# Kernel optimization log

Hardware: AMD Instinct MI355X
Metric: run time of the kernel (lower is better)

The kernel has to match this reference:

```python
import jax, jax.numpy as jnp
import numpy as np

B, T, C = 4, 2048, 1024
QH = 4            # n_q_heads
D = C // QH       # per-head dim = 256
EPS = 1e-5


def setup_inputs() -> dict:
    key = jax.random.key(0)
    k1, k2, k3 = jax.random.split(key, 3)
    residual = jax.random.normal(k1, (B, T, C), dtype=jnp.float32)
    # scale weights ~ Xavier-ish so relu(score)^2 stays numerically sane
    w_fc = jax.random.normal(k2, (C, C), dtype=jnp.float32) * (1.0 / np.sqrt(C))
    w_proj = jax.random.normal(k3, (C, C), dtype=jnp.float32) * (1.0 / np.sqrt(C))
    ln_g = jnp.ones((C,), dtype=jnp.float32)
    ln_b = jnp.zeros((C,), dtype=jnp.float32)
    return {"residual": residual, "w_fc": w_fc, "w_proj": w_proj,
            "ln_g": ln_g, "ln_b": ln_b}


def _layernorm(x, g, b):
    mu = jnp.mean(x, axis=-1, keepdims=True)
    var = jnp.mean(jnp.square(x - mu), axis=-1, keepdims=True)
    return (x - mu) * jax.lax.rsqrt(var + EPS) * g + b


def reference(residual, w_fc, w_proj, ln_g, ln_b):
    Bx, Tx, Cx = residual.shape
    x = _layernorm(residual, ln_g, ln_b)
    # q: (B, QH, T, D)
    q = x.reshape(Bx, Tx, QH, D).transpose(0, 2, 1, 3)
    # keys: rows of w_fc chopped into 4C kv entries of dim D, shared across heads
    k = w_fc.reshape(-1, D)          # (S, D), S = 4C
    # values: columns of w_proj (i.e. w_proj^T rows) chopped the same way
    v = w_proj.T.reshape(-1, D)      # (S, D)
    scores = jnp.einsum('bhtd,sd->bhts', q, k)
    # softmax(log(relusq(score))) then *exp(lse) == plain relu(score)^2 weights
    p = jnp.square(jax.nn.relu(scores))
    out = jnp.einsum('bhts,sd->bhtd', p, v)
    out = out.transpose(0, 2, 1, 3).reshape(Bx, Tx, Cx)
    return residual + out
```

## Files before the change

### kernel.cpp

```cpp
#include <hip/hip_runtime.h>
#include <hip/hip_bf16.h>

typedef __attribute__((ext_vector_type(8))) short bf16x8;
typedef __attribute__((ext_vector_type(4))) float f32x4;

#define C_    1024
#define MROWS 32768
#define D_    256
#define S_TOT 4096
#define SCH   32
#define NCH   (S_TOT / SCH)

__device__ __forceinline__ unsigned short f2bf(float f) {
  union { float f; unsigned int u; } v; v.f = f;
  unsigned int u = v.u;
  u += 0x7fffu + ((u >> 16) & 1u);
  return (unsigned short)(u >> 16);
}

__device__ __forceinline__ void async16(const void* g, void* l) {
  __builtin_amdgcn_global_load_lds(
      (const __attribute__((address_space(1))) unsigned int*)g,
      (__attribute__((address_space(3))) unsigned int*)l, 16, 0, 0);
}

__global__ __launch_bounds__(256) void ln_kernel(const float* __restrict__ res,
                                                 const float* __restrict__ g,
                                                 const float* __restrict__ b,
                                                 unsigned short* __restrict__ xq) {
  int wave = threadIdx.x >> 6, lane = threadIdx.x & 63;
  int row = blockIdx.x * 4 + wave;
  const float* r = res + (size_t)row * C_;
  float4 x[4];
  float s = 0.f, s2 = 0.f;
  #pragma unroll
  for (int i = 0; i < 4; ++i) {
    x[i] = *(const float4*)(r + i * 256 + lane * 4);
    s  += x[i].x + x[i].y + x[i].z + x[i].w;
    s2 += x[i].x * x[i].x + x[i].y * x[i].y + x[i].z * x[i].z + x[i].w * x[i].w;
  }
  #pragma unroll
  for (int off = 32; off > 0; off >>= 1) {
    s  += __shfl_xor(s, off, 64);
    s2 += __shfl_xor(s2, off, 64);
  }
  float mu  = s * (1.0f / C_);
  float var = s2 * (1.0f / C_) - mu * mu;
  float rs  = rsqrtf(var + 1e-5f);
  #pragma unroll
  for (int i = 0; i < 4; ++i) {
    int c = i * 256 + lane * 4;
    float4 gg = *(const float4*)(g + c);
    float4 bb = *(const float4*)(b + c);
    unsigned short o[4];
    o[0] = f2bf((x[i].x - mu) * rs * gg.x + bb.x);
    o[1] = f2bf((x[i].y - mu) * rs * gg.y + bb.y);
    o[2] = f2bf((x[i].z - mu) * rs * gg.z + bb.z);
    o[3] = f2bf((x[i].w - mu) * rs * gg.w + bb.w);
    *(ushort4*)(xq + (size_t)row * C_ + c) = *(ushort4*)o;
  }
}

__global__ __launch_bounds__(256) void prep_k(const float* __restrict__ wfc,
                                              unsigned short* __restrict__ kq) {
  int t = blockIdx.x * 256 + threadIdx.x;
  int lane = t & 63;
  int sn  = (t >> 6) & 1;
  int kc  = (t >> 7) & 7;
  int sc2 = t >> 10;
  int s = sc2 * 32 + sn * 16 + (lane & 15);
  int d = kc * 32 + (lane >> 4) * 8;
  const float* src = wfc + (size_t)s * D_ + d;
  float4 a = *(const float4*)src;
  float4 b = *(const float4*)(src + 4);
  unsigned short o[8] = { f2bf(a.x), f2bf(a.y), f2bf(a.z), f2bf(a.w),
                          f2bf(b.x), f2bf(b.y), f2bf(b.z), f2bf(b.w) };
  *(uint4*)(kq + (size_t)t * 8) = *(uint4*)o;
}

__global__ __launch_bounds__(256) void prep_v(const float* __restrict__ wproj,
                                              unsigned short* __restrict__ vq) {
  __shared__ unsigned short tile[8192];
  int b = blockIdx.x;
  int tid = threadIdx.x;
  int c0 = b * 8;
  #pragma unroll
  for (int it = 0; it < 4; ++it) {
    int row = it * 256 + tid;
    const float* src = wproj + (size_t)row * C_ + c0;
    float4 a = *(const float4*)src;
    float4 bb = *(const float4*)(src + 4);
    unsigned short* dst = &tile[row * 8];
    dst[0] = f2bf(a.x);  dst[1] = f2bf(a.y);  dst[2] = f2bf(a.z);  dst[3] = f2bf(a.w);
    dst[4] = f2bf(bb.x); dst[5] = f2bf(bb.y); dst[6] = f2bf(bb.z); dst[7] = f2bf(bb.w);
  }
  __syncthreads();
  #pragma unroll
  for (int it = 0; it < 4; ++it) {
    int slot = it * 256 + tid;
    int lane = slot & 63;
    int dn   = slot >> 6;
    int d = dn * 16 + (lane & 15);
    int sl0 = (lane >> 4) * 8;
    unsigned short o[8];
    #pragma unroll
    for (int j = 0; j < 8; ++j) {
      int sl = sl0 + j;
      o[j] = tile[((sl & 3) * 256 + d) * 8 + (sl >> 2)];
    }
    *(uint4*)(vq + (size_t)b * 8192 + (size_t)slot * 8) = *(uint4*)o;
  }
}

__global__ __launch_bounds__(512, 2) void mlpmha_main(
    const unsigned short* __restrict__ xq,
    const unsigned short* __restrict__ kq,
    const unsigned short* __restrict__ vq,
    const float* __restrict__ res,
    float* __restrict__ out) {
  __shared__ unsigned short ldsK[2][8192];
  __shared__ unsigned short ldsV[8192];
  __shared__ unsigned short ldsP[128][36];

  int tid  = threadIdx.x;
  int wave = tid >> 6;
  int lane = tid & 63;
  int l16  = lane & 15;
  int quad = lane >> 4;
  int wgM  = blockIdx.x * 128;

  int mi = wave & 3, si = wave >> 2;
  int ni = wave & 3, mi2 = wave >> 2;

  bf16x8 qf[2][8];
  #pragma unroll
  for (int mt = 0; mt < 2; ++mt) {
    const unsigned short* qr =
        xq + (size_t)(wgM + mi * 32 + mt * 16 + l16) * D_ + quad * 8;
    #pragma unroll
    for (int kc = 0; kc < 8; ++kc) qf[mt][kc] = *(const bf16x8*)(qr + kc * 32);
  }

  f32x4 acc[4][4];
  #pragma unroll
  for (int i = 0; i < 4; ++i)
    #pragma unroll
    for (int j = 0; j < 4; ++j) acc[i][j] = (f32x4){0.f, 0.f, 0.f, 0.f};

  int soff = tid * 8;

  {
    const unsigned short* kg = kq + soff;
    async16(kg, &ldsK[0][soff]);
    async16(kg + 4096, &ldsK[0][soff + 4096]);
  }
  __syncthreads();

  for (int sc = 0; sc < NCH; ++sc) {
    int cur = sc & 1;

    {
      const unsigned short* vg = vq + (size_t)sc * 8192 + soff;
      async16(vg, &ldsV[soff]);
      async16(vg + 4096, &ldsV[soff + 4096]);
    }

    f32x4 sacc[2];
    sacc[0] = (f32x4){0.f, 0.f, 0.f, 0.f};
    sacc[1] = (f32x4){0.f, 0.f, 0.f, 0.f};
    #pragma unroll
    for (int kc = 0; kc < 8; ++kc) {
      bf16x8 kb = *(const bf16x8*)&ldsK[cur][(kc * 2 + si) * 512 + lane * 8];
      #pragma unroll
      for (int mt = 0; mt < 2; ++mt)
        sacc[mt] = __builtin_amdgcn_mfma_f32_16x16x32_bf16(qf[mt][kc], kb, sacc[mt], 0, 0, 0);
    }

    #pragma unroll
    for (int mt = 0; mt < 2; ++mt)
      #pragma unroll
      for (int r = 0; r < 4; ++r) {
        float v = sacc[mt][r];
        v = v > 0.f ? v * v : 0.f;
        ldsP[mi * 32 + mt * 16 + quad * 4 + r][si * 16 + l16] = f2bf(v);
      }

    __syncthreads();

    if (sc + 1 < NCH) {
      const unsigned short* kg = kq + (size_t)(sc + 1) * 8192 + soff;
      async16(kg, &ldsK[1 - cur][soff]);
      async16(kg + 4096, &ldsK[1 - cur][soff + 4096]);
    }

    {
      bf16x8 vb[4];
      #pragma unroll
      for (int dnl = 0; dnl < 4; ++dnl)
        vb[dnl] = *(const bf16x8*)&ldsV[((ni * 4 + dnl) * 64 + lane) * 8];
      #pragma unroll
      for (int mt2 = 0; mt2 < 4; ++mt2) {
        const unsigned short* pp = &ldsP[mi2 * 64 + mt2 * 16 + l16][quad * 8];
        union { ushort4 h[2]; bf16x8 v; } pu;
        pu.h[0] = *(const ushort4*)pp;
        pu.h[1] = *(const ushort4*)(pp + 4);
        bf16x8 pa = pu.v;
        #pragma unroll
        for (int dnl = 0; dnl < 4; ++dnl)
          acc[mt2][dnl] = __builtin_amdgcn_mfma_f32_16x16x32_bf16(pa, vb[dnl], acc[mt2][dnl], 0, 0, 0);
      }
    }

    __syncthreads();
  }

  #pragma unroll
  for (int mt2 = 0; mt2 < 4; ++mt2)
    #pragma unroll
    for (int r = 0; r < 4; ++r) {
      size_t row = (size_t)(wgM + mi2 * 64 + mt2 * 16 + quad * 4 + r) * D_;
      #pragma unroll
      for (int dnl = 0; dnl < 4; ++dnl) {
        size_t idx = row + ni * 64 + dnl * 16 + l16;
        out[idx] = res[idx] + acc[mt2][dnl][r];
      }
    }
}

extern "C" void kernel_launch(void* const* d_in, const int* in_sizes, int n_in,
                              void* d_out, int out_size, void* d_ws, size_t ws_size,
                              hipStream_t stream) {
  const float* res   = (const float*)d_in[0];
  const float* wfc   = (const float*)d_in[1];
  const float* wproj = (const float*)d_in[2];
  const float* g     = (const float*)d_in[3];
  const float* b     = (const float*)d_in[4];
  float* out = (float*)d_out;

  unsigned short* xq = (unsigned short*)d_ws;
  unsigned short* kq = xq + (size_t)MROWS * D_;
  unsigned short* vq = kq + (size_t)S_TOT * D_;

  ln_kernel<<<2048, 256, 0, stream>>>(res, g, b, xq);
  prep_k<<<512, 256, 0, stream>>>(wfc, kq);
  prep_v<<<128, 256, 0, stream>>>(wproj, vq);
  mlpmha_main<<<256, 512, 0, stream>>>(xq, kq, vq, res, out);
}
```

Before: 243.0 us.

## Software-pipeline scores and PV phases with triple-buffered P and register V

Restructures the main loop so the score MFMA for chunk s+1 overlaps the P·V MFMA for chunk s. P gets three LDS buffers, which cuts the loop to one barrier per chunk instead of two. V fragments are loaded straight from global memory into registers, double-buffered, instead of being staged through LDS. This is meant to remove barrier stalls and LDS traffic, at the cost of more registers and V reads from global/L2 that are exposed to latency.

```diff
diff --git a/kernel.cpp b/kernel.cpp
--- a/kernel.cpp
+++ b/kernel.cpp
@@ -119,8 +119,7 @@
     const float* __restrict__ res,
     float* __restrict__ out) {
   __shared__ unsigned short ldsK[2][8192];
-  __shared__ unsigned short ldsV[8192];
-  __shared__ unsigned short ldsP[128][36];
+  __shared__ unsigned short ldsP[3][128][36];
 
   int tid  = threadIdx.x;
   int wave = tid >> 6;
@@ -149,22 +148,23 @@
 
   int soff = tid * 8;
 
-  {
-    const unsigned short* kg = kq + soff;
-    async16(kg, &ldsK[0][soff]);
-    async16(kg + 4096, &ldsK[0][soff + 4096]);
-  }
-  __syncthreads();
-
-  for (int sc = 0; sc < NCH; ++sc) {
+  bf16x8 vbA[4], vbB[4];
+
+  auto load_v = [&](int sc, bf16x8 (&vb)[4]) {
+    const unsigned short* vg = vq + (size_t)sc * 8192;
+    #pragma unroll
+    for (int dnl = 0; dnl < 4; ++dnl)
+      vb[dnl] = *(const bf16x8*)(vg + ((ni * 4 + dnl) * 64 + lane) * 8);
+  };
+
+  auto issueK = [&](int sc, int buf) {
+    const unsigned short* kg = kq + (size_t)sc * 8192 + soff;
+    async16(kg, &ldsK[buf][soff]);
+    async16(kg + 4096, &ldsK[buf][soff + 4096]);
+  };
+
+  auto scores_phase = [&](int sc, int pw) {
     int cur = sc & 1;
-
-    {
-      const unsigned short* vg = vq + (size_t)sc * 8192 + soff;
-      async16(vg, &ldsV[soff]);
-      async16(vg + 4096, &ldsV[soff + 4096]);
-    }
-
     f32x4 sacc[2];
     sacc[0] = (f32x4){0.f, 0.f, 0.f, 0.f};
     sacc[1] = (f32x4){0.f, 0.f, 0.f, 0.f};
@@ -175,44 +175,63 @@
       for (int mt = 0; mt < 2; ++mt)
         sacc[mt] = __builtin_amdgcn_mfma_f32_16x16x32_bf16(qf[mt][kc], kb, sacc[mt], 0, 0, 0);
     }
-
     #pragma unroll
     for (int mt = 0; mt < 2; ++mt)
       #pragma unroll
       for (int r = 0; r < 4; ++r) {
         float v = sacc[mt][r];
         v = v > 0.f ? v * v : 0.f;
-        ldsP[mi * 32 + mt * 16 + quad * 4 + r][si * 16 + l16] = f2bf(v);
+        ldsP[pw][mi * 32 + mt * 16 + quad * 4 + r][si * 16 + l16] = f2bf(v);
       }
-
+  };
+
+  auto pv_phase = [&](int pr, bf16x8 (&vb)[4]) {
+    #pragma unroll
+    for (int mt2 = 0; mt2 < 4; ++mt2) {
+      const unsigned short* pp = &ldsP[pr][mi2 * 64 + mt2 * 16 + l16][quad * 8];
+      union { ushort4 h[2]; bf16x8 v; } pu;
+      pu.h[0] = *(const ushort4*)pp;
+      pu.h[1] = *(const ushort4*)(pp + 4);
+      bf16x8 pa = pu.v;
+      #pragma unroll
+      for (int dnl = 0; dnl < 4; ++dnl)
+        acc[mt2][dnl] = __builtin_amdgcn_mfma_f32_16x16x32_bf16(pa, vb[dnl], acc[mt2][dnl], 0, 0, 0);
+    }
+  };
+
+  issueK(0, 0);
+  issueK(1, 1);
+  load_v(0, vbA);
+  __syncthreads();
+
+  scores_phase(0, 0);
+  __syncthreads();
+  issueK(2, 0);
+
+  int prev = 0;
+  int nxt  = 1;
+
+  for (int sc = 1; sc < NCH - 1; sc += 2) {
+    load_v(sc, vbB);
+    scores_phase(sc, nxt);
     __syncthreads();
-
-    if (sc + 1 < NCH) {
-      const unsigned short* kg = kq + (size_t)(sc + 1) * 8192 + soff;
-      async16(kg, &ldsK[1 - cur][soff]);
-      async16(kg + 4096, &ldsK[1 - cur][soff + 4096]);
-    }
-
-    {
-      bf16x8 vb[4];
-      #pragma unroll
-      for (int dnl = 0; dnl < 4; ++dnl)
-        vb[dnl] = *(const bf16x8*)&ldsV[((ni * 4 + dnl) * 64 + lane) * 8];
-      #pragma unroll
-      for (int mt2 = 0; mt2 < 4; ++mt2) {
-        const unsigned short* pp = &ldsP[mi2 * 64 + mt2 * 16 + l16][quad * 8];
-        union { ushort4 h[2]; bf16x8 v; } pu;
-        pu.h[0] = *(const ushort4*)pp;
-        pu.h[1] = *(const ushort4*)(pp + 4);
-        bf16x8 pa = pu.v;
-        #pragma unroll
-        for (int dnl = 0; dnl < 4; ++dnl)
-          acc[mt2][dnl] = __builtin_amdgcn_mfma_f32_16x16x32_bf16(pa, vb[dnl], acc[mt2][dnl], 0, 0, 0);
-      }
-    }
-
+    issueK(sc + 2, 1);
+    pv_phase(prev, vbA);
+    prev = nxt; nxt = (nxt == 2) ? 0 : nxt + 1;
+
+    load_v(sc + 1, vbA);
+    scores_phase(sc + 1, nxt);
     __syncthreads();
-  }
+    if (sc + 3 < NCH) issueK(sc + 3, 0);
+    pv_phase(prev, vbB);
+    prev = nxt; nxt = (nxt == 2) ? 0 : nxt + 1;
+  }
+
+  load_v(NCH - 1, vbB);
+  scores_phase(NCH - 1, nxt);
+  __syncthreads();
+  pv_phase(prev, vbA);
+  pv_phase(nxt, vbB);
 
   #pragma unroll
   for (int mt2 = 0; mt2 < 4; ++mt2)
```

After: 260.3 us. 7.1% more time.

## Software-pipeline score and PV stages with double-buffered V and P

Applied to the files above, without the earlier changes.

The main loop is restructured so that each iteration computes the relu-squared scores for chunk sc while running the P·V MFMAs for chunk sc-1. V and P tiles are now double-buffered in LDS, with a prologue and epilogue added, which cuts the loop to one barrier per iteration instead of two. The aim is to overlap LDS loads, score MFMAs and PV MFMAs and to hide the async loads. In exchange, register pressure rises because the pa and vb fragments stay live across the score phase, and LDS per block grows, which could limit occupancy.

```diff
diff --git a/kernel.cpp b/kernel.cpp
--- a/kernel.cpp
+++ b/kernel.cpp
@@ -119,8 +119,8 @@
     const float* __restrict__ res,
     float* __restrict__ out) {
   __shared__ unsigned short ldsK[2][8192];
-  __shared__ unsigned short ldsV[8192];
-  __shared__ unsigned short ldsP[128][36];
+  __shared__ unsigned short ldsV[2][8192];
+  __shared__ unsigned short ldsP[2][128][36];
 
   int tid  = threadIdx.x;
   int wave = tid >> 6;
@@ -149,69 +149,110 @@
 
   int soff = tid * 8;
 
+  auto issueK = [&](int sc, int buf) {
+    const unsigned short* kg = kq + (size_t)sc * 8192 + soff;
+    async16(kg, &ldsK[buf][soff]);
+    async16(kg + 4096, &ldsK[buf][soff + 4096]);
+  };
+  auto issueV = [&](int sc, int buf) {
+    const unsigned short* vg = vq + (size_t)sc * 8192 + soff;
+    async16(vg, &ldsV[buf][soff]);
+    async16(vg + 4096, &ldsV[buf][soff + 4096]);
+  };
+
+  issueK(0, 0);
+  __syncthreads();
+
+  issueK(1, 1);
+  issueV(0, 0);
   {
-    const unsigned short* kg = kq + soff;
-    async16(kg, &ldsK[0][soff]);
-    async16(kg + 4096, &ldsK[0][soff + 4096]);
-  }
-  __syncthreads();
-
-  for (int sc = 0; sc < NCH; ++sc) {
-    int cur = sc & 1;
-
-    {
-      const unsigned short* vg = vq + (size_t)sc * 8192 + soff;
-      async16(vg, &ldsV[soff]);
-      async16(vg + 4096, &ldsV[soff + 4096]);
-    }
-
     f32x4 sacc[2];
     sacc[0] = (f32x4){0.f, 0.f, 0.f, 0.f};
     sacc[1] = (f32x4){0.f, 0.f, 0.f, 0.f};
     #pragma unroll
     for (int kc = 0; kc < 8; ++kc) {
-      bf16x8 kb = *(const bf16x8*)&ldsK[cur][(kc * 2 + si) * 512 + lane * 8];
+      bf16x8 kb = *(const bf16x8*)&ldsK[0][(kc * 2 + si) * 512 + lane * 8];
       #pragma unroll
       for (int mt = 0; mt < 2; ++mt)
         sacc[mt] = __builtin_amdgcn_mfma_f32_16x16x32_bf16(qf[mt][kc], kb, sacc[mt], 0, 0, 0);
     }
-
     #pragma unroll
     for (int mt = 0; mt < 2; ++mt)
       #pragma unroll
       for (int r = 0; r < 4; ++r) {
         float v = sacc[mt][r];
         v = v > 0.f ? v * v : 0.f;
-        ldsP[mi * 32 + mt * 16 + quad * 4 + r][si * 16 + l16] = f2bf(v);
+        ldsP[0][mi * 32 + mt * 16 + quad * 4 + r][si * 16 + l16] = f2bf(v);
       }
+  }
+  __syncthreads();
+
+  for (int sc = 1; sc < NCH; ++sc) {
+    int cur = sc & 1;
+    int prv = 1 - cur;
+
+    if (sc + 1 < NCH) issueK(sc + 1, prv);
+    issueV(sc, cur);
+
+    bf16x8 vb[4];
+    #pragma unroll
+    for (int dnl = 0; dnl < 4; ++dnl)
+      vb[dnl] = *(const bf16x8*)&ldsV[prv][((ni * 4 + dnl) * 64 + lane) * 8];
+    bf16x8 pa[4];
+    #pragma unroll
+    for (int mt2 = 0; mt2 < 4; ++mt2) {
+      const unsigned short* pp = &ldsP[prv][mi2 * 64 + mt2 * 16 + l16][quad * 8];
+      union { ushort4 h[2]; bf16x8 v; } pu;
+      pu.h[0] = *(const ushort4*)pp;
+      pu.h[1] = *(const ushort4*)(pp + 4);
+      pa[mt2] = pu.v;
+    }
+
+    f32x4 sacc[2];
+    sacc[0] = (f32x4){0.f, 0.f, 0.f, 0.f};
+    sacc[1] = (f32x4){0.f, 0.f, 0.f, 0.f};
+    #pragma unroll
+    for (int kc = 0; kc < 8; ++kc) {
+      bf16x8 kb = *(const bf16x8*)&ldsK[cur][(kc * 2 + si) * 512 + lane * 8];
+      #pragma unroll
+      for (int mt = 0; mt < 2; ++mt)
+        sacc[mt] = __builtin_amdgcn_mfma_f32_16x16x32_bf16(qf[mt][kc], kb, sacc[mt], 0, 0, 0);
+    }
+
+    #pragma unroll
+    for (int mt = 0; mt < 2; ++mt)
+      #pragma unroll
+      for (int r = 0; r < 4; ++r) {
+        float v = sacc[mt][r];
+        v = v > 0.f ? v * v : 0.f;
+        ldsP[cur][mi * 32 + mt * 16 + quad * 4 + r][si * 16 + l16] = f2bf(v);
+      }
+
+    #pragma unroll
+    for (int mt2 = 0; mt2 < 4; ++mt2)
+      #pragma unroll
+      for (int dnl = 0; dnl < 4; ++dnl)
+        acc[mt2][dnl] = __builtin_amdgcn_mfma_f32_16x16x32_bf16(pa[mt2], vb[dnl], acc[mt2][dnl], 0, 0, 0);
 
     __syncthreads();
-
-    if (sc + 1 < NCH) {
-      const unsigned short* kg = kq + (size_t)(sc + 1) * 8192 + soff;
-      async16(kg, &ldsK[1 - cur][soff]);
-      async16(kg + 4096, &ldsK[1 - cur][soff + 4096]);
-    }
-
-    {
-      bf16x8 vb[4];
+  }
+
+  {
+    bf16x8 vb[4];
+    #pragma unroll
+    for (int dnl = 0; dnl < 4; ++dnl)
+      vb[dnl] = *(const bf16x8*)&ldsV[1][((ni * 4 + dnl) * 64 + lane) * 8];
+    #pragma unroll
+    for (int mt2 = 0; mt2 < 4; ++mt2) {
+      const unsigned short* pp = &ldsP[1][mi2 * 64 + mt2 * 16 + l16][quad * 8];
+      union { ushort4 h[2]; bf16x8 v; } pu;
+      pu.h[0] = *(const ushort4*)pp;
+      pu.h[1] = *(const ushort4*)(pp + 4);
+      bf16x8 pa = pu.v;
       #pragma unroll
       for (int dnl = 0; dnl < 4; ++dnl)
-        vb[dnl] = *(const bf16x8*)&ldsV[((ni * 4 + dnl) * 64 + lane) * 8];
-      #pragma unroll
-      for (int mt2 = 0; mt2 < 4; ++mt2) {
-        const unsigned short* pp = &ldsP[mi2 * 64 + mt2 * 16 + l16][quad * 8];
-        union { ushort4 h[2]; bf16x8 v; } pu;
-        pu.h[0] = *(const ushort4*)pp;
-        pu.h[1] = *(const ushort4*)(pp + 4);
-        bf16x8 pa = pu.v;
-        #pragma unroll
-        for (int dnl = 0; dnl < 4; ++dnl)
-          acc[mt2][dnl] = __builtin_amdgcn_mfma_f32_16x16x32_bf16(pa, vb[dnl], acc[mt2][dnl], 0, 0, 0);
-      }
-    }
-
-    __syncthreads();
+        acc[mt2][dnl] = __builtin_amdgcn_mfma_f32_16x16x32_bf16(pa, vb[dnl], acc[mt2][dnl], 0, 0, 0);
+    }
   }
 
   #pragma unroll
```

After: 299.5 us. +23.2%, slower.

## Warp-specialize main kernel into score and PV wave groups with double buffering

Applied to the files above, without the earlier changes.

Splits the 8 waves of the main kernel into two roles. Waves 0-3 compute relu² scores for chunk s, while waves 4-7 run the P·V MFMAs for chunk s-1. The chunk size doubles to 64 keys, V and P become double-buffered, and the P tile uses an XOR-swizzled layout to reduce LDS bank conflicts. The aim is to overlap the two GEMM phases and halve the number of barriers per key. The cost is about 160KB of LDS, which limits each CU to one workgroup, plus larger accumulator register pressure.

```diff
diff --git a/kernel.cpp b/kernel.cpp
--- a/kernel.cpp
+++ b/kernel.cpp
@@ -8,8 +8,9 @@
 #define MROWS 32768
 #define D_    256
 #define S_TOT 4096
-#define SCH   32
+#define SCH   64
 #define NCH   (S_TOT / SCH)
+#define CHW   16384
 
 __device__ __forceinline__ unsigned short f2bf(float f) {
   union { float f; unsigned int u; } v; v.f = f;
@@ -118,9 +119,9 @@
     const unsigned short* __restrict__ vq,
     const float* __restrict__ res,
     float* __restrict__ out) {
-  __shared__ unsigned short ldsK[2][8192];
-  __shared__ unsigned short ldsV[8192];
-  __shared__ unsigned short ldsP[128][36];
+  __shared__ unsigned short ldsK[2][CHW];
+  __shared__ unsigned short ldsV[2][CHW];
+  __shared__ unsigned short ldsP[2][8192];
 
   int tid  = threadIdx.x;
   int wave = tid >> 6;
@@ -129,102 +130,125 @@
   int quad = lane >> 4;
   int wgM  = blockIdx.x * 128;
 
-  int mi = wave & 3, si = wave >> 2;
-  int ni = wave & 3, mi2 = wave >> 2;
-
-  bf16x8 qf[2][8];
-  #pragma unroll
-  for (int mt = 0; mt < 2; ++mt) {
-    const unsigned short* qr =
-        xq + (size_t)(wgM + mi * 32 + mt * 16 + l16) * D_ + quad * 8;
-    #pragma unroll
-    for (int kc = 0; kc < 8; ++kc) qf[mt][kc] = *(const bf16x8*)(qr + kc * 32);
-  }
-
-  f32x4 acc[4][4];
+  int soff = tid * 8;
+
+  auto issue32 = [&](const unsigned short* gbase, unsigned short* lbase) {
+    #pragma unroll
+    for (int seg = 0; seg < 4; ++seg)
+      async16(gbase + soff + seg * 4096, lbase + soff + seg * 4096);
+  };
+
+  int miP = (wave >> 1) & 1;
+  int sg  = wave & 1;
+  bf16x8 qf[4][8];
+  if (wave < 4) {
+    #pragma unroll
+    for (int mt = 0; mt < 4; ++mt) {
+      const unsigned short* qr =
+          xq + (size_t)(wgM + miP * 64 + mt * 16 + l16) * D_ + quad * 8;
+      #pragma unroll
+      for (int kc = 0; kc < 8; ++kc) qf[mt][kc] = *(const bf16x8*)(qr + kc * 32);
+    }
+  }
+
+  int cw  = wave - 4;
+  int mi2 = (cw >> 1) & 1;
+  int ni  = cw & 1;
+  f32x4 acc[4][8];
   #pragma unroll
   for (int i = 0; i < 4; ++i)
     #pragma unroll
-    for (int j = 0; j < 4; ++j) acc[i][j] = (f32x4){0.f, 0.f, 0.f, 0.f};
-
-  int soff = tid * 8;
-
-  {
-    const unsigned short* kg = kq + soff;
-    async16(kg, &ldsK[0][soff]);
-    async16(kg + 4096, &ldsK[0][soff + 4096]);
-  }
+    for (int j = 0; j < 8; ++j) acc[i][j] = (f32x4){0.f, 0.f, 0.f, 0.f};
+
+  auto scores_do = [&](const unsigned short* kbuf, unsigned short* pbuf) {
+    f32x4 sacc[4][2];
+    #pragma unroll
+    for (int mt = 0; mt < 4; ++mt) {
+      sacc[mt][0] = (f32x4){0.f, 0.f, 0.f, 0.f};
+      sacc[mt][1] = (f32x4){0.f, 0.f, 0.f, 0.f};
+    }
+    const unsigned short* kb_base = kbuf + sg * 8192 + lane * 8;
+    #pragma unroll
+    for (int kc = 0; kc < 8; ++kc) {
+      bf16x8 kb0 = *(const bf16x8*)(kb_base + (kc * 2 + 0) * 512);
+      bf16x8 kb1 = *(const bf16x8*)(kb_base + (kc * 2 + 1) * 512);
+      #pragma unroll
+      for (int mt = 0; mt < 4; ++mt) {
+        sacc[mt][0] = __builtin_amdgcn_mfma_f32_16x16x32_bf16(qf[mt][kc], kb0, sacc[mt][0], 0, 0, 0);
+        sacc[mt][1] = __builtin_amdgcn_mfma_f32_16x16x32_bf16(qf[mt][kc], kb1, sacc[mt][1], 0, 0, 0);
+      }
+    }
+    #pragma unroll
+    for (int mt = 0; mt < 4; ++mt)
+      #pragma unroll
+      for (int st = 0; st < 2; ++st)
+        #pragma unroll
+        for (int r = 0; r < 4; ++r) {
+          float v = sacc[mt][st][r];
+          v = v > 0.f ? v * v : 0.f;
+          int row = miP * 64 + mt * 16 + quad * 4 + r;
+          int col = sg * 32 + st * 16 + l16;
+          pbuf[(row * 64 + col) ^ ((row & 7) << 3)] = f2bf(v);
+        }
+  };
+
+  auto pv_do = [&](const unsigned short* pbuf, const unsigned short* vbuf) {
+    #pragma unroll
+    for (int ks = 0; ks < 2; ++ks) {
+      bf16x8 pa[4];
+      #pragma unroll
+      for (int mt2 = 0; mt2 < 4; ++mt2) {
+        int row = mi2 * 64 + mt2 * 16 + l16;
+        pa[mt2] = *(const bf16x8*)(pbuf + ((row * 64 + ks * 32 + quad * 8) ^ ((row & 7) << 3)));
+      }
+      bf16x8 vb[8];
+      #pragma unroll
+      for (int dnl = 0; dnl < 8; ++dnl)
+        vb[dnl] = *(const bf16x8*)(vbuf + ks * 8192 + ((ni * 8 + dnl) * 64 + lane) * 8);
+      #pragma unroll
+      for (int mt2 = 0; mt2 < 4; ++mt2)
+        #pragma unroll
+        for (int dnl = 0; dnl < 8; ++dnl)
+          acc[mt2][dnl] = __builtin_amdgcn_mfma_f32_16x16x32_bf16(pa[mt2], vb[dnl], acc[mt2][dnl], 0, 0, 0);
+    }
+  };
+
+  issue32(kq, ldsK[0]);
   __syncthreads();
 
-  for (int sc = 0; sc < NCH; ++sc) {
+  issue32(kq + CHW, ldsK[1]);
+  issue32(vq, ldsV[0]);
+  if (wave < 4) scores_do(ldsK[0], ldsP[0]);
+  __syncthreads();
+
+  for (int sc = 1; sc < NCH; ++sc) {
     int cur = sc & 1;
-
-    {
-      const unsigned short* vg = vq + (size_t)sc * 8192 + soff;
-      async16(vg, &ldsV[soff]);
-      async16(vg + 4096, &ldsV[soff + 4096]);
-    }
-
-    f32x4 sacc[2];
-    sacc[0] = (f32x4){0.f, 0.f, 0.f, 0.f};
-    sacc[1] = (f32x4){0.f, 0.f, 0.f, 0.f};
-    #pragma unroll
-    for (int kc = 0; kc < 8; ++kc) {
-      bf16x8 kb = *(const bf16x8*)&ldsK[cur][(kc * 2 + si) * 512 + lane * 8];
-      #pragma unroll
-      for (int mt = 0; mt < 2; ++mt)
-        sacc[mt] = __builtin_amdgcn_mfma_f32_16x16x32_bf16(qf[mt][kc], kb, sacc[mt], 0, 0, 0);
-    }
-
-    #pragma unroll
-    for (int mt = 0; mt < 2; ++mt)
+    int prv = 1 - cur;
+    if (sc + 1 < NCH) issue32(kq + (size_t)(sc + 1) * CHW, ldsK[1 - cur]);
+    issue32(vq + (size_t)sc * CHW, ldsV[cur]);
+    if (wave < 4) {
+      scores_do(ldsK[cur], ldsP[cur]);
+    } else {
+      pv_do(ldsP[prv], ldsV[prv]);
+    }
+    __syncthreads();
+  }
+
+  if (wave >= 4) pv_do(ldsP[1], ldsV[1]);
+
+  if (wave >= 4) {
+    #pragma unroll
+    for (int mt2 = 0; mt2 < 4; ++mt2)
       #pragma unroll
       for (int r = 0; r < 4; ++r) {
-        float v = sacc[mt][r];
-        v = v > 0.f ? v * v : 0.f;
-        ldsP[mi * 32 + mt * 16 + quad * 4 + r][si * 16 + l16] = f2bf(v);
+        size_t row = (size_t)(wgM + mi2 * 64 + mt2 * 16 + quad * 4 + r) * D_;
+        #pragma unroll
+        for (int dnl = 0; dnl < 8; ++dnl) {
+          size_t idx = row + ni * 128 + dnl * 16 + l16;
+          out[idx] = res[idx] + acc[mt2][dnl][r];
+        }
       }
-
-    __syncthreads();
-
-    if (sc + 1 < NCH) {
-      const unsigned short* kg = kq + (size_t)(sc + 1) * 8192 + soff;
-      async16(kg, &ldsK[1 - cur][soff]);
-      async16(kg + 4096, &ldsK[1 - cur][soff + 4096]);
-    }
-
-    {
-      bf16x8 vb[4];
-      #pragma unroll
-      for (int dnl = 0; dnl < 4; ++dnl)
-        vb[dnl] = *(const bf16x8*)&ldsV[((ni * 4 + dnl) * 64 + lane) * 8];
-      #pragma unroll
-      for (int mt2 = 0; mt2 < 4; ++mt2) {
-        const unsigned short* pp = &ldsP[mi2 * 64 + mt2 * 16 + l16][quad * 8];
-        union { ushort4 h[2]; bf16x8 v; } pu;
-        pu.h[0] = *(const ushort4*)pp;
-        pu.h[1] = *(const ushort4*)(pp + 4);
-        bf16x8 pa = pu.v;
-        #pragma unroll
-        for (int dnl = 0; dnl < 4; ++dnl)
-          acc[mt2][dnl] = __builtin_amdgcn_mfma_f32_16x16x32_bf16(pa, vb[dnl], acc[mt2][dnl], 0, 0, 0);
-      }
-    }
-
-    __syncthreads();
-  }
-
-  #pragma unroll
-  for (int mt2 = 0; mt2 < 4; ++mt2)
-    #pragma unroll
-    for (int r = 0; r < 4; ++r) {
-      size_t row = (size_t)(wgM + mi2 * 64 + mt2 * 16 + quad * 4 + r) * D_;
-      #pragma unroll
-      for (int dnl = 0; dnl < 4; ++dnl) {
-        size_t idx = row + ni * 64 + dnl * 16 + l16;
-        out[idx] = res[idx] + acc[mt2][dnl][r];
-      }
-    }
+  }
 }
 
 extern "C" void kernel_launch(void* const* d_in, const int* in_sizes, int n_in,
```

After: 857.8 us. +253.0%, slower.
